# Kernel optimization log

Hardware: AMD Instinct MI355X
Metric: run time of the kernel (lower is better)

Reference implementation:

```python
import jax, jax.numpy as jnp
import numpy as np

N, C, H, E = 51200, 200, 128, 8
NE = N * 32
S_COEF, B_COEF = 0.01, 0.01
BN_EPS = 1e-5


def setup_inputs() -> dict:
    key = jax.random.key(0)
    ks = jax.random.split(key, 12)
    inp = {}
    inp["v"] = jax.random.normal(ks[0], (N, C), jnp.float32)
    inp["a_rows"] = jax.random.randint(ks[1], (NE,), 0, N, dtype=jnp.int32)
    inp["a_cols"] = jax.random.randint(ks[2], (NE,), 0, N, dtype=jnp.int32)
    inp["a_vals"] = jax.random.uniform(ks[3], (NE,), jnp.float32)
    inp["gate_W"] = jax.random.normal(ks[4], (C, E), jnp.float32) * 0.05
    inp["gate_b"] = jnp.zeros((E,), jnp.float32)
    inp["eps"] = jnp.zeros((E,), jnp.float32)  # GIN epsilon, init 0
    inp["W1"] = jax.random.normal(ks[5], (E, C, H), jnp.float32) / np.sqrt(C)
    inp["b1"] = jnp.zeros((E, H), jnp.float32)
    inp["g1"] = jnp.ones((E, H), jnp.float32)
    inp["beta1"] = jnp.zeros((E, H), jnp.float32)
    inp["W2"] = jax.random.normal(ks[6], (E, H, H), jnp.float32) / np.sqrt(H)
    inp["b2"] = jnp.zeros((E, H), jnp.float32)
    inp["g2"] = jnp.ones((E, H), jnp.float32)
    inp["beta2"] = jnp.zeros((E, H), jnp.float32)
    inp["b"] = 4
    inp["t"] = 64
    inp["n"] = 200
    return inp


def _bn_relu(h, g, beta):
    # h: [E, N, H]; batch-norm over node axis per expert (training-mode batch stats)
    mu = jnp.mean(h, axis=1, keepdims=True)
    var = jnp.var(h, axis=1, keepdims=True)
    hn = (h - mu) * jax.lax.rsqrt(var + BN_EPS)
    return jax.nn.relu(hn * g[:, None, :] + beta[:, None, :])


def reference(v, a_rows, a_cols, a_vals, gate_W, gate_b, eps,
              W1, b1, g1, beta1, W2, b2, g2, beta2, b, t, n):
    num_nodes, c = v.shape
    e = gate_W.shape[1]
    # ---- gating on x = rearrange(v, '(b t n) c -> b t n c') ----
    x = v.reshape(b, t, n, c)
    logits = jnp.einsum('btnc,ce->btne', x, gate_W) + gate_b
    probs = jax.nn.softmax(logits, axis=-1)                 # [b,t,n,E]
    top_val = jnp.max(probs, axis=-1, keepdims=True)
    top_idx = jnp.argmax(probs, axis=-1)
    gates = jax.nn.one_hot(top_idx, e, dtype=probs.dtype) * top_val  # top-1 sparse gates
    # ---- aux losses (switch-style balance; sparsity = mean top prob) ----
    probs_flat = probs.reshape(-1, e)
    gates_flat = gates.reshape(-1, e)
    importance = jnp.mean(probs_flat, axis=0)
    load = jnp.mean(jax.nn.one_hot(top_idx.reshape(-1), e, dtype=probs.dtype), axis=0)
    bal_loss = B_COEF * e * jnp.sum(importance * load)
    spa_loss = -S_COEF * jnp.mean(top_val)
    # ---- all-expert GIN compute (dense over experts, as in the torch loop) ----
    # shared sparse aggregation: agg[i] = sum_j a[i,j] * v[j]
    agg = jax.ops.segment_sum(a_vals[:, None] * v[a_cols], a_rows, num_segments=num_nodes)
    xin = agg[None] + (1.0 + eps)[:, None, None] * v[None]  # [E,N,C]
    h = jnp.einsum('enc,ech->enh', xin, W1) + b1[:, None, :]
    h = _bn_relu(h, g1, beta1)
    h = jnp.einsum('enk,ekh->enh', h, W2) + b2[:, None, :]
    h = _bn_relu(h, g2, beta2)                               # [E,N,H]
    # ---- gate-masked combine ----
    out = jnp.einsum('enh,ne->nh', h, gates_flat)            # [N,H]
    return out, (bal_loss, spa_loss)
```

## Files before the change

### kernel.cpp

```cpp
#include <hip/hip_runtime.h>


#define NNODES 51200
#define CDIM   200
#define CPAD   208
#define HDIM   128
#define NEXP   8
#define BNEPS  1e-5f
#define KC1    26
#define KS2    8
#define NB     400
#define CAP    6144
#define EPB    8192

typedef __attribute__((ext_vector_type(8)))  short short8;
typedef __attribute__((ext_vector_type(16))) float floatx16;
typedef unsigned short ushort_t;

__device__ __forceinline__ ushort_t f2bf(float x) {
  unsigned int u = __float_as_uint(x);
  u += 0x7fffu + ((u >> 16) & 1u);
  return (ushort_t)(u >> 16);
}
__device__ __forceinline__ float bf2f(ushort_t h) {
  return __uint_as_float(((unsigned int)h) << 16);
}

__global__ __launch_bounds__(256) void gating_kernel(
    const float* __restrict__ v, const float* __restrict__ gW,
    const float* __restrict__ gb, int* __restrict__ top_idx,
    float* __restrict__ top_val, ushort_t* __restrict__ v_bf,
    float* __restrict__ imp_acc, float* __restrict__ cnt_acc,
    float* __restrict__ tv_acc)
{
  __shared__ float s_imp[NEXP], s_cnt[NEXP], s_tv;
  const int tid = threadIdx.x, lane = tid & 63, wave = tid >> 6;
  if (tid < NEXP) { s_imp[tid] = 0.f; s_cnt[tid] = 0.f; }
  if (tid == 0) s_tv = 0.f;
  __syncthreads();
  const int c0 = lane * 4;
  const bool act = lane < 50;
  float gwr[4][NEXP];
#pragma unroll
  for (int r = 0; r < 4; ++r)
#pragma unroll
    for (int e = 0; e < NEXP; ++e)
      gwr[r][e] = act ? gW[(c0 + r) * NEXP + e] : 0.f;
  for (int i = 0; i < 16; ++i) {
    const int node = blockIdx.x * 64 + wave * 16 + i;
    float4 x = make_float4(0.f, 0.f, 0.f, 0.f);
    if (act) x = *(const float4*)(v + (size_t)node * CDIM + c0);
    float p[NEXP];
#pragma unroll
    for (int e = 0; e < NEXP; ++e)
      p[e] = fmaf(x.x, gwr[0][e],
             fmaf(x.y, gwr[1][e],
             fmaf(x.z, gwr[2][e], x.w * gwr[3][e])));
#pragma unroll
    for (int off = 32; off > 0; off >>= 1)
#pragma unroll
      for (int e = 0; e < NEXP; ++e) p[e] += __shfl_xor(p[e], off, 64);
#pragma unroll
    for (int e = 0; e < NEXP; ++e) p[e] += gb[e];
    if (lane < 52) {
      ushort4 o = {0, 0, 0, 0};
      if (act) { o.x = f2bf(x.x); o.y = f2bf(x.y); o.z = f2bf(x.z); o.w = f2bf(x.w); }
      *(ushort4*)(v_bf + (size_t)node * CPAD + c0) = o;
    }
    float mx = p[0]; int ai = 0;
#pragma unroll
    for (int e = 1; e < NEXP; ++e) if (p[e] > mx) { mx = p[e]; ai = e; }
    float se = 0.f, pe[NEXP];
#pragma unroll
    for (int e = 0; e < NEXP; ++e) { pe[e] = __expf(p[e] - mx); se += pe[e]; }
    const float inv = 1.f / se;
    if (lane == 0) {
      top_idx[node] = ai;
      top_val[node] = inv;
#pragma unroll
      for (int e = 0; e < NEXP; ++e) atomicAdd(&s_imp[e], pe[e] * inv);
      atomicAdd(&s_cnt[ai], 1.f);
      atomicAdd(&s_tv, inv);
    }
  }
  __syncthreads();
  if (tid < NEXP) { atomicAdd(&imp_acc[tid], s_imp[tid]); atomicAdd(&cnt_acc[tid], s_cnt[tid]); }
  if (tid == 0) atomicAdd(tv_acc, s_tv);
}

__global__ __launch_bounds__(256) void bucketA_kernel(
    const int* __restrict__ rows, const int* __restrict__ cols,
    const float* __restrict__ vals, int* __restrict__ bcnt,
    int2* __restrict__ tmp, int ne)
{
  __shared__ int cnt[NB];
  __shared__ int gbase[NB];
  const int tid = threadIdx.x;
  const int base = blockIdx.x * EPB;
  for (int b = tid; b < NB; b += 256) cnt[b] = 0;
  __syncthreads();
#pragma unroll 4
  for (int j = 0; j < EPB / 256; ++j) {
    const int i = base + j * 256 + tid;
    if (i < ne) atomicAdd(&cnt[rows[i] >> 7], 1);
  }
  __syncthreads();
  for (int b = tid; b < NB; b += 256) {
    const int c = cnt[b];
    gbase[b] = c ? (b * CAP + atomicAdd(&bcnt[b], c)) : 0;
    cnt[b] = 0;
  }
  __syncthreads();
#pragma unroll 4
  for (int j = 0; j < EPB / 256; ++j) {
    const int i = base + j * 256 + tid;
    if (i < ne) {
      const int r = rows[i];
      const int b = r >> 7;
      const int pos = gbase[b] + atomicAdd(&cnt[b], 1);
      tmp[pos] = make_int2((r << 16) | cols[i], __float_as_int(vals[i]));
    }
  }
}

__global__ __launch_bounds__(256) void bucketB_kernel(
    const int2* __restrict__ tmp, const int* __restrict__ bcnt,
    int2* __restrict__ cv, int* __restrict__ row_start, int* __restrict__ counts)
{
  __shared__ int lhist[128];
  __shared__ int lcur[128];
  const int tid = threadIdx.x;
  const int b = blockIdx.x;
  const int n = bcnt[b];
  const int base = b * CAP;
  int2 ed[CAP / 256];
#pragma unroll
  for (int j = 0; j < CAP / 256; ++j) {
    const int i = j * 256 + tid;
    if (i < n) ed[j] = tmp[base + i];
  }
  if (tid < 128) lhist[tid] = 0;
  __syncthreads();
#pragma unroll
  for (int j = 0; j < CAP / 256; ++j)
    if (j * 256 + tid < n)
      atomicAdd(&lhist[(((unsigned)ed[j].x) >> 16) & 127], 1);
  __syncthreads();
  if (tid == 0) {
    int acc = base;
    for (int r = 0; r < 128; ++r) { lcur[r] = acc; acc += lhist[r]; }
  }
  __syncthreads();
  if (tid < 128) {
    row_start[(b << 7) + tid] = lcur[tid];
    counts[(b << 7) + tid] = lhist[tid];
  }
  __syncthreads();
#pragma unroll
  for (int j = 0; j < CAP / 256; ++j)
    if (j * 256 + tid < n) {
      const int r = (((unsigned)ed[j].x) >> 16) & 127;
      const int pos = atomicAdd(&lcur[r], 1);
      cv[pos] = make_int2(ed[j].x & 0xffff, ed[j].y);
    }
}

__global__ __launch_bounds__(256) void aggregate_kernel(
    const ushort_t* __restrict__ v_bf, const int2* __restrict__ cv,
    const int* __restrict__ row_start, const int* __restrict__ counts,
    ushort_t* __restrict__ agg_bf)
{
  const int node = (blockIdx.x * 256 + threadIdx.x) >> 6;
  const int lane = threadIdx.x & 63;
  const int half = lane >> 5;
  const int l32  = lane & 31;
  const bool act = l32 < 26;
  const int start = row_start[node];
  const int cnt   = counts[node];

  float acc[8];
#pragma unroll
  for (int j = 0; j < 8; ++j) acc[j] = 0.f;

  int ecol = 0, eval = 0;
  if (lane < cnt) {
    const int2 e = cv[start + lane];
    ecol = e.x; eval = e.y;
  }
  const int n64 = cnt < 64 ? cnt : 64;
  int k = 0;

  for (; k + 16 <= n64; k += 16) {
    short8 xx[8];
#pragma unroll
    for (int u = 0; u < 8; ++u) {
      const int cc = __shfl(ecol, k + 2 * u + half, 64);
      short8 t = {0, 0, 0, 0, 0, 0, 0, 0};
      if (act) t = *(const short8*)(v_bf + (size_t)cc * CPAD + l32 * 8);
      xx[u] = t;
    }
#pragma unroll
    for (int u = 0; u < 8; ++u) {
      const float vv = __int_as_float(__shfl(eval, k + 2 * u + half, 64));
#pragma unroll
      for (int j = 0; j < 8; ++j)
        acc[j] = fmaf(vv, bf2f((ushort_t)xx[u][j]), acc[j]);
    }
  }
  for (; k + 4 <= n64; k += 4) {
    short8 xx[2];
#pragma unroll
    for (int u = 0; u < 2; ++u) {
      const int cc = __shfl(ecol, k + 2 * u + half, 64);
      short8 t = {0, 0, 0, 0, 0, 0, 0, 0};
      if (act) t = *(const short8*)(v_bf + (size_t)cc * CPAD + l32 * 8);
      xx[u] = t;
    }
#pragma unroll
    for (int u = 0; u < 2; ++u) {
      const float vv = __int_as_float(__shfl(eval, k + 2 * u + half, 64));
#pragma unroll
      for (int j = 0; j < 8; ++j)
        acc[j] = fmaf(vv, bf2f((ushort_t)xx[u][j]), acc[j]);
    }
  }
  for (; k < n64; k += 2) {
    const int idx = k + half;
    const int cc = __shfl(ecol, idx, 64);
    short8 t = {0, 0, 0, 0, 0, 0, 0, 0};
    if (act) t = *(const short8*)(v_bf + (size_t)cc * CPAD + l32 * 8);
    const float vv = __int_as_float(__shfl(eval, idx, 64));
#pragma unroll
    for (int j = 0; j < 8; ++j)
      acc[j] = fmaf(vv, bf2f((ushort_t)t[j]), acc[j]);
  }
  for (; k < cnt; ++k) {
    const int2 e0 = cv[start + k];
    short8 x0 = {0, 0, 0, 0, 0, 0, 0, 0};
    if (act && half == 0)
      x0 = *(const short8*)(v_bf + (size_t)e0.x * CPAD + l32 * 8);
    const float v0 = half ? 0.f : __int_as_float(e0.y);
#pragma unroll
    for (int j = 0; j < 8; ++j)
      acc[j] = fmaf(v0, bf2f((ushort_t)x0[j]), acc[j]);
  }

#pragma unroll
  for (int j = 0; j < 8; ++j) acc[j] += __shfl_xor(acc[j], 32, 64);

  if (act && half == 0) {
    short8 o;
#pragma unroll
    for (int j = 0; j < 8; ++j) o[j] = (short)f2bf(acc[j]);
    *(short8*)(agg_bf + (size_t)node * CPAD + l32 * 8) = o;
  }
}

__global__ __launch_bounds__(256) void btconv_all(
    const float* __restrict__ W1, const float* __restrict__ W2,
    const float* __restrict__ eps, ushort_t* __restrict__ Bt1,
    ushort_t* __restrict__ Bt2)
{
  const int e = blockIdx.y, j = blockIdx.x;
  __shared__ float tile[16][128];
  const int tid = threadIdx.x;
  const int kr = tid >> 5, n4 = (tid & 31) * 4;
  const float* W; int K, jj; float sc; ushort_t* dst;
  if (j < KC1) {
    sc = (j >= 13) ? (1.f + eps[e]) : 1.f;
    jj = (j >= 13) ? (j - 13) : j;
    W = W1; K = CDIM;
    dst = Bt1 + (((size_t)e * KC1 + j) * 256) * 8;
  } else {
    sc = 1.f; jj = j - KC1; W = W2; K = HDIM;
    dst = Bt2 + (((size_t)e * KS2 + jj) * 256) * 8;
  }
#pragma unroll
  for (int h = 0; h < 2; ++h) {
    const int k = jj * 16 + kr + h * 8;
    float4 val = make_float4(0.f, 0.f, 0.f, 0.f);
    if (k < K) val = *(const float4*)(W + ((size_t)e * K + k) * HDIM + n4);
    *(float4*)&tile[kr + h * 8][n4] = val;
  }
  __syncthreads();
  const int kh = tid >> 7, n = tid & 127;
  short8 pk;
#pragma unroll
  for (int q = 0; q < 8; ++q) pk[q] = (short)f2bf(sc * tile[kh * 8 + q][n]);
  *(short8*)(dst + (size_t)tid * 8) = pk;
}

__global__ __launch_bounds__(256, 2) void gemm1_mfma(
    const ushort_t* __restrict__ agg_bf, const ushort_t* __restrict__ v_bf,
    const ushort_t* __restrict__ Bt1x, ushort_t* __restrict__ h1,
    float* __restrict__ sum1, float* __restrict__ sq1)
{
  const int m0 = blockIdx.x * 64;
  __shared__ ushort_t sA[52 * 64 * 8];
  const int tid = threadIdx.x;
  const int lane = tid & 63, wid = tid >> 6;
  const int l31 = lane & 31, half = lane >> 5;

#pragma unroll
  for (int it = 0; it < 13; ++it) {
    const int l = it * 256 + tid;
    const int g = l >> 6, m = l & 63;
    const ushort_t* src = (g < 26)
        ? agg_bf + (size_t)(m0 + m) * CPAD + g * 8
        : v_bf  + (size_t)(m0 + m) * CPAD + (g - 26) * 8;
    *(short8*)(sA + (size_t)l * 8) = *(const short8*)src;
  }
  __syncthreads();

#pragma unroll
  for (int ei = 0; ei < 2; ++ei) {
    const int e = wid + ei * 4;
    floatx16 acc[2][4];
#pragma unroll
    for (int ms = 0; ms < 2; ++ms)
#pragma unroll
      for (int ns = 0; ns < 4; ++ns)
#pragma unroll
        for (int r = 0; r < 16; ++r) acc[ms][ns][r] = 0.f;

    const ushort_t* bte = Bt1x + ((size_t)e * KC1 * 256 + half * 128 + l31) * 8;
    short8 nb[4];
#pragma unroll
    for (int ns = 0; ns < 4; ++ns)
      nb[ns] = *(const short8*)(bte + (size_t)(ns * 32) * 8);
#pragma unroll
    for (int j = 0; j < KC1; ++j) {
      short8 b[4];
#pragma unroll
      for (int ns = 0; ns < 4; ++ns) b[ns] = nb[ns];
      if (j < KC1 - 1) {
#pragma unroll
        for (int ns = 0; ns < 4; ++ns)
          nb[ns] = *(const short8*)(bte + (size_t)((j + 1) * 256 + ns * 32) * 8);
      }
      short8 a[2];
#pragma unroll
      for (int ms = 0; ms < 2; ++ms)
        a[ms] = *(const short8*)(sA + (size_t)((2 * j + half) * 64 + ms * 32 + l31) * 8);
#pragma unroll
      for (int ms = 0; ms < 2; ++ms)
#pragma unroll
        for (int ns = 0; ns < 4; ++ns)
          acc[ms][ns] = __builtin_amdgcn_mfma_f32_32x32x16_bf16(
              a[ms], b[ns], acc[ms][ns], 0, 0, 0);
    }

    ushort_t* h1e = h1 + ((size_t)e * NNODES + m0) * HDIM;
#pragma unroll
    for (int ns = 0; ns < 4; ++ns) {
      const int col = ns * 32 + l31;
      float s = 0.f, q = 0.f;
#pragma unroll
      for (int ms = 0; ms < 2; ++ms) {
#pragma unroll
        for (int r = 0; r < 16; ++r) {
          const int row = ms * 32 + (r & 3) + 8 * (r >> 2) + 4 * half;
          const float x = acc[ms][ns][r];
          h1e[(size_t)row * HDIM + col] = f2bf(x);
          s += x; q = fmaf(x, x, q);
        }
      }
      s += __shfl_xor(s, 32, 64);
      q += __shfl_xor(q, 32, 64);
      if (half == 0) {
        atomicAdd(&sum1[e * HDIM + col], s);
        atomicAdd(&sq1[e * HDIM + col], q);
      }
    }
  }
}

__global__ __launch_bounds__(256, 4) void gemm2_mfma(
    const ushort_t* __restrict__ h1, const ushort_t* __restrict__ Bt2,
    const float* __restrict__ sum1, const float* __restrict__ sq1,
    const float* __restrict__ g1, const float* __restrict__ beta1,
    const int* __restrict__ top_idx, float* __restrict__ h2_sel,
    float* __restrict__ sum2, float* __restrict__ sq2)
{
  const int e = blockIdx.y;
  const int m0 = blockIdx.x * 128;
  __shared__ ushort_t sA[16 * 129 * 8];
  __shared__ float ssum[HDIM], ssq[HDIM];
  __shared__ float sSc[HDIM], sSh[HDIM];
  __shared__ int sTop[128];
  const int tid = threadIdx.x;
  const int lane = tid & 63, wid = tid >> 6;
  const int wm = wid >> 1, wn = wid & 1;
  const int l31 = lane & 31, half = lane >> 5;
  if (tid < HDIM) {
    ssum[tid] = 0.f; ssq[tid] = 0.f;
    sTop[tid] = top_idx[m0 + tid];
    const int i = e * HDIM + tid;
    const float invN = 1.f / (float)NNODES;
    const float mean = sum1[i] * invN;
    const float var  = sq1[i] * invN - mean * mean;
    const float sc = rsqrtf(var + BNEPS) * g1[i];
    sSc[tid] = sc;
    sSh[tid] = fmaf(-mean, sc, beta1[i]);
  }
  __syncthreads();
  {
    const int g = tid & 15, r0 = tid >> 4;
    const float4 sc0 = *(const float4*)&sSc[g * 8];
    const float4 sc1 = *(const float4*)&sSc[g * 8 + 4];
    const float4 sh0 = *(const float4*)&sSh[g * 8];
    const float4 sh1 = *(const float4*)&sSh[g * 8 + 4];
#pragma unroll
    for (int c = 0; c < 8; ++c) {
      const int m = c * 16 + r0;
      const short8 hq = *(const short8*)(
          h1 + ((size_t)e * NNODES + m0 + m) * HDIM + g * 8);
      short8 pk;
      pk[0] = (short)f2bf(fmaxf(0.f, fmaf(bf2f((ushort_t)hq[0]), sc0.x, sh0.x)));
      pk[1] = (short)f2bf(fmaxf(0.f, fmaf(bf2f((ushort_t)hq[1]), sc0.y, sh0.y)));
      pk[2] = (short)f2bf(fmaxf(0.f, fmaf(bf2f((ushort_t)hq[2]), sc0.z, sh0.z)));
      pk[3] = (short)f2bf(fmaxf(0.f, fmaf(bf2f((ushort_t)hq[3]), sc0.w, sh0.w)));
      pk[4] = (short)f2bf(fmaxf(0.f, fmaf(bf2f((ushort_t)hq[4]), sc1.x, sh1.x)));
      pk[5] = (short)f2bf(fmaxf(0.f, fmaf(bf2f((ushort_t)hq[5]), sc1.y, sh1.y)));
      pk[6] = (short)f2bf(fmaxf(0.f, fmaf(bf2f((ushort_t)hq[6]), sc1.z, sh1.z)));
      pk[7] = (short)f2bf(fmaxf(0.f, fmaf(bf2f((ushort_t)hq[7]), sc1.w, sh1.w)));
      *(short8*)(sA + (size_t)(g * 129 + m) * 8) = pk;
    }
  }
  __syncthreads();

  floatx16 acc[2][2];
#pragma unroll
  for (int i = 0; i < 2; ++i)
#pragma unroll
    for (int j = 0; j < 2; ++j)
#pragma unroll
      for (int r = 0; r < 16; ++r) acc[i][j][r] = 0.f;

  const ushort_t* bte = Bt2 + ((size_t)e * KS2 * 256 + half * 128 + wn * 64 + l31) * 8;
  short8 nb0 = *(const short8*)(bte);
  short8 nb1 = *(const short8*)(bte + 32 * 8);
#pragma unroll
  for (int ks = 0; ks < KS2; ++ks) {
    const short8 b0 = nb0, b1 = nb1;
    if (ks < KS2 - 1) {
      nb0 = *(const short8*)(bte + (size_t)((ks + 1) * 256) * 8);
      nb1 = *(const short8*)(bte + (size_t)((ks + 1) * 256 + 32) * 8);
    }
    const short8 a0 = *(const short8*)(sA + (size_t)((2 * ks + half) * 129 + wm * 64 + l31) * 8);
    const short8 a1 = *(const short8*)(sA + (size_t)((2 * ks + half) * 129 + wm * 64 + 32 + l31) * 8);
    acc[0][0] = __builtin_amdgcn_mfma_f32_32x32x16_bf16(a0, b0, acc[0][0], 0, 0, 0);
    acc[0][1] = __builtin_amdgcn_mfma_f32_32x32x16_bf16(a0, b1, acc[0][1], 0, 0, 0);
    acc[1][0] = __builtin_amdgcn_mfma_f32_32x32x16_bf16(a1, b0, acc[1][0], 0, 0, 0);
    acc[1][1] = __builtin_amdgcn_mfma_f32_32x32x16_bf16(a1, b1, acc[1][1], 0, 0, 0);
  }

#pragma unroll
  for (int ms = 0; ms < 2; ++ms)
#pragma unroll
    for (int ns = 0; ns < 2; ++ns) {
      const int col = wn * 64 + ns * 32 + l31;
      float s = 0.f, q = 0.f;
#pragma unroll
      for (int r = 0; r < 16; ++r) {
        const int row = wm * 64 + ms * 32 + (r & 3) + 8 * (r >> 2) + 4 * half;
        const float x = acc[ms][ns][r];
        if (sTop[row] == e) h2_sel[(size_t)(m0 + row) * HDIM + col] = x;
        s += x; q = fmaf(x, x, q);
      }
      atomicAdd(&ssum[col], s);
      atomicAdd(&ssq[col], q);
    }
  __syncthreads();
  if (tid < HDIM) atomicAdd(&sum2[e * HDIM + tid], ssum[tid]);
  else            atomicAdd(&sq2[e * HDIM + tid - HDIM], ssq[tid - HDIM]);
}

__global__ __launch_bounds__(256) void combine_kernel(
    const float* __restrict__ h2_sel, const int* __restrict__ top_idx,
    const float* __restrict__ top_val, const float* __restrict__ sum2,
    const float* __restrict__ sq2, const float* __restrict__ g2,
    const float* __restrict__ beta2, const float* __restrict__ imp,
    const float* __restrict__ cntv, const float* __restrict__ tv,
    float* __restrict__ out)
{
  __shared__ float s2[NEXP * HDIM], b2s[NEXP * HDIM];
  const int tid = threadIdx.x;
  const float invN = 1.f / (float)NNODES;
  for (int t = tid; t < NEXP * HDIM; t += 256) {
    const float mean = sum2[t] * invN;
    const float var  = sq2[t] * invN - mean * mean;
    const float sc = rsqrtf(var + BNEPS) * g2[t];
    s2[t] = sc;
    b2s[t] = fmaf(-mean, sc, beta2[t]);
  }
  __syncthreads();
  const int i4 = (blockIdx.x * 256 + tid) * 4;
  const int n = i4 >> 7, h = i4 & 127;
  const int e = top_idx[n];
  const float tvv = top_val[n];
  const float4 x = *(const float4*)(h2_sel + i4);
  const float* sc = s2 + e * HDIM + h;
  const float* sh = b2s + e * HDIM + h;
  float4 o;
  o.x = tvv * fmaxf(0.f, fmaf(x.x, sc[0], sh[0]));
  o.y = tvv * fmaxf(0.f, fmaf(x.y, sc[1], sh[1]));
  o.z = tvv * fmaxf(0.f, fmaf(x.z, sc[2], sh[2]));
  o.w = tvv * fmaxf(0.f, fmaf(x.w, sc[3], sh[3]));
  *(float4*)(out + i4) = o;
  if (blockIdx.x == 0 && tid == 0) {
    float bal = 0.f;
#pragma unroll
    for (int q = 0; q < NEXP; ++q) bal += (imp[q] * invN) * (cntv[q] * invN);
    out[(size_t)NNODES * HDIM]     = 0.01f * (float)NEXP * bal;
    out[(size_t)NNODES * HDIM + 1] = -0.01f * tv[0] * invN;
  }
}

struct WS {
  ushort_t *v_bf, *agg_bf, *h1, *Bt1x, *Bt2;
  float *h2_sel;
  int2 *cv, *tmp;
  int *row_start, *counts, *top_idx;
  float *top_val;
  char *zero_base; size_t zero_bytes;
  int *bcnt;
  float *sum1, *sq1, *sum2, *sq2, *imp, *cnt, *tv;
  size_t total;
};

static WS carve_ws(char* base)
{
  WS w; size_t off = 0;
  auto take = [&](size_t b) -> char* {
    char* r = base + off; off += (b + 255) & ~(size_t)255; return r;
  };
  w.v_bf   = (ushort_t*)take((size_t)NNODES * CPAD * 2);
  w.agg_bf = (ushort_t*)take((size_t)NNODES * CPAD * 2);
  w.h2_sel = (float*)w.v_bf;
  w.h1     = (ushort_t*)take((size_t)NEXP * NNODES * HDIM * 2);
  w.cv     = (int2*)take((size_t)NB * CAP * 8);
  w.tmp    = (int2*)take((size_t)NB * CAP * 8);
  w.Bt1x   = (ushort_t*)take((size_t)NEXP * KC1 * 2048 * 2);
  w.Bt2    = (ushort_t*)take((size_t)NEXP * KS2 * 2048 * 2);
  w.row_start = (int*)take(NNODES * 4);
  w.counts    = (int*)take(NNODES * 4);
  w.top_idx   = (int*)take(NNODES * 4);
  w.top_val   = (float*)take(NNODES * 4);
  w.zero_base = base + off;
  w.bcnt = (int*)take(NB * 4);
  w.sum1 = (float*)take(NEXP * HDIM * 4);
  w.sq1  = (float*)take(NEXP * HDIM * 4);
  w.sum2 = (float*)take(NEXP * HDIM * 4);
  w.sq2  = (float*)take(NEXP * HDIM * 4);
  w.imp  = (float*)take(NEXP * 4);
  w.cnt  = (float*)take(NEXP * 4);
  w.tv   = (float*)take(4);
  w.zero_bytes = (size_t)((base + off) - w.zero_base);
  w.total = off;
  return w;
}

extern "C" void kernel_launch(void* const* d_in, const int* in_sizes, int n_in,
                              void* d_out, int out_size, void* d_ws, size_t ws_size,
                              hipStream_t stream)
{
  const float* v      = (const float*)d_in[0];
  const int*   a_rows = (const int*)d_in[1];
  const int*   a_cols = (const int*)d_in[2];
  const float* a_vals = (const float*)d_in[3];
  const float* gate_W = (const float*)d_in[4];
  const float* gate_b = (const float*)d_in[5];
  const float* eps    = (const float*)d_in[6];
  const float* W1     = (const float*)d_in[7];
  const float* g1     = (const float*)d_in[9];
  const float* beta1  = (const float*)d_in[10];
  const float* W2     = (const float*)d_in[11];
  const float* g2     = (const float*)d_in[13];
  const float* beta2  = (const float*)d_in[14];
  const int NE = in_sizes[1];
  float* out = (float*)d_out;
  (void)n_in; (void)out_size; (void)ws_size;

  WS w = carve_ws((char*)d_ws);

  hipMemsetAsync(w.zero_base, 0, w.zero_bytes, stream);

  gating_kernel<<<NNODES / 64, 256, 0, stream>>>(
      v, gate_W, gate_b, w.top_idx, w.top_val, w.v_bf, w.imp, w.cnt, w.tv);
  btconv_all<<<dim3(KC1 + KS2, NEXP), 256, 0, stream>>>(
      W1, W2, eps, w.Bt1x, w.Bt2);
  bucketA_kernel<<<(NE + EPB - 1) / EPB, 256, 0, stream>>>(
      a_rows, a_cols, a_vals, w.bcnt, w.tmp, NE);
  bucketB_kernel<<<NB, 256, 0, stream>>>(
      w.tmp, w.bcnt, w.cv, w.row_start, w.counts);
  aggregate_kernel<<<NNODES / 4, 256, 0, stream>>>(
      w.v_bf, w.cv, w.row_start, w.counts, w.agg_bf);

  gemm1_mfma<<<NNODES / 64, 256, 0, stream>>>(
      w.agg_bf, w.v_bf, w.Bt1x, w.h1, w.sum1, w.sq1);
  gemm2_mfma<<<dim3(NNODES / 128, NEXP), 256, 0, stream>>>(
      w.h1, w.Bt2, w.sum1, w.sq1, g1, beta1, w.top_idx,
      w.h2_sel, w.sum2, w.sq2);
  combine_kernel<<<(NNODES * HDIM) / 1024, 256, 0, stream>>>(
      w.h2_sel, w.top_idx, w.top_val, w.sum2, w.sq2, g2, beta2,
      w.imp, w.cnt, w.tv, out);
}
```

Measured before the change: 517.7 us.

## Fuse sparse neighbor aggregation into gemm1 prologue, dropping agg buffer

The separate aggregate kernel is removed. gemm1 now gathers and sums neighbor rows of v_bf directly into its shared-memory A tile, each wave handling 16 nodes with the next node's edge list prefetched. This avoids writing and re-reading the bf16 agg array and one kernel launch. The cost is that the gather latency now sits inside the GEMM kernel, which runs at only 800 blocks with a 2-blocks-per-CU bound, so it has less parallelism to hide irregular memory accesses. The workspace for v_bf is also resized so it can still alias h2_sel.

```diff
diff --git a/kernel.cpp b/kernel.cpp
--- a/kernel.cpp
+++ b/kernel.cpp
@@ -163,97 +163,6 @@
       const int pos = atomicAdd(&lcur[r], 1);
       cv[pos] = make_int2(ed[j].x & 0xffff, ed[j].y);
     }
-}
-
-__global__ __launch_bounds__(256) void aggregate_kernel(
-    const ushort_t* __restrict__ v_bf, const int2* __restrict__ cv,
-    const int* __restrict__ row_start, const int* __restrict__ counts,
-    ushort_t* __restrict__ agg_bf)
-{
-  const int node = (blockIdx.x * 256 + threadIdx.x) >> 6;
-  const int lane = threadIdx.x & 63;
-  const int half = lane >> 5;
-  const int l32  = lane & 31;
-  const bool act = l32 < 26;
-  const int start = row_start[node];
-  const int cnt   = counts[node];
-
-  float acc[8];
-#pragma unroll
-  for (int j = 0; j < 8; ++j) acc[j] = 0.f;
-
-  int ecol = 0, eval = 0;
-  if (lane < cnt) {
-    const int2 e = cv[start + lane];
-    ecol = e.x; eval = e.y;
-  }
-  const int n64 = cnt < 64 ? cnt : 64;
-  int k = 0;
-
-  for (; k + 16 <= n64; k += 16) {
-    short8 xx[8];
-#pragma unroll
-    for (int u = 0; u < 8; ++u) {
-      const int cc = __shfl(ecol, k + 2 * u + half, 64);
-      short8 t = {0, 0, 0, 0, 0, 0, 0, 0};
-      if (act) t = *(const short8*)(v_bf + (size_t)cc * CPAD + l32 * 8);
-      xx[u] = t;
-    }
-#pragma unroll
-    for (int u = 0; u < 8; ++u) {
-      const float vv = __int_as_float(__shfl(eval, k + 2 * u + half, 64));
-#pragma unroll
-      for (int j = 0; j < 8; ++j)
-        acc[j] = fmaf(vv, bf2f((ushort_t)xx[u][j]), acc[j]);
-    }
-  }
-  for (; k + 4 <= n64; k += 4) {
-    short8 xx[2];
-#pragma unroll
-    for (int u = 0; u < 2; ++u) {
-      const int cc = __shfl(ecol, k + 2 * u + half, 64);
-      short8 t = {0, 0, 0, 0, 0, 0, 0, 0};
-      if (act) t = *(const short8*)(v_bf + (size_t)cc * CPAD + l32 * 8);
-      xx[u] = t;
-    }
-#pragma unroll
-    for (int u = 0; u < 2; ++u) {
-      const float vv = __int_as_float(__shfl(eval, k + 2 * u + half, 64));
-#pragma unroll
-      for (int j = 0; j < 8; ++j)
-        acc[j] = fmaf(vv, bf2f((ushort_t)xx[u][j]), acc[j]);
-    }
-  }
-  for (; k < n64; k += 2) {
-    const int idx = k + half;
-    const int cc = __shfl(ecol, idx, 64);
-    short8 t = {0, 0, 0, 0, 0, 0, 0, 0};
-    if (act) t = *(const short8*)(v_bf + (size_t)cc * CPAD + l32 * 8);
-    const float vv = __int_as_float(__shfl(eval, idx, 64));
-#pragma unroll
-    for (int j = 0; j < 8; ++j)
-      acc[j] = fmaf(vv, bf2f((ushort_t)t[j]), acc[j]);
-  }
-  for (; k < cnt; ++k) {
-    const int2 e0 = cv[start + k];
-    short8 x0 = {0, 0, 0, 0, 0, 0, 0, 0};
-    if (act && half == 0)
-      x0 = *(const short8*)(v_bf + (size_t)e0.x * CPAD + l32 * 8);
-    const float v0 = half ? 0.f : __int_as_float(e0.y);
-#pragma unroll
-    for (int j = 0; j < 8; ++j)
-      acc[j] = fmaf(v0, bf2f((ushort_t)x0[j]), acc[j]);
-  }
-
-#pragma unroll
-  for (int j = 0; j < 8; ++j) acc[j] += __shfl_xor(acc[j], 32, 64);
-
-  if (act && half == 0) {
-    short8 o;
-#pragma unroll
-    for (int j = 0; j < 8; ++j) o[j] = (short)f2bf(acc[j]);
-    *(short8*)(agg_bf + (size_t)node * CPAD + l32 * 8) = o;
-  }
 }
 
 __global__ __launch_bounds__(256) void btconv_all(
@@ -291,7 +200,8 @@
 }
 
 __global__ __launch_bounds__(256, 2) void gemm1_mfma(
-    const ushort_t* __restrict__ agg_bf, const ushort_t* __restrict__ v_bf,
+    const ushort_t* __restrict__ v_bf, const int2* __restrict__ cv,
+    const int* __restrict__ row_start, const int* __restrict__ counts,
     const ushort_t* __restrict__ Bt1x, ushort_t* __restrict__ h1,
     float* __restrict__ sum1, float* __restrict__ sq1)
 {
@@ -302,13 +212,109 @@
   const int l31 = lane & 31, half = lane >> 5;
 
 #pragma unroll
-  for (int it = 0; it < 13; ++it) {
+  for (int it = 0; it < 7; ++it) {
     const int l = it * 256 + tid;
-    const int g = l >> 6, m = l & 63;
-    const ushort_t* src = (g < 26)
-        ? agg_bf + (size_t)(m0 + m) * CPAD + g * 8
-        : v_bf  + (size_t)(m0 + m) * CPAD + (g - 26) * 8;
-    *(short8*)(sA + (size_t)l * 8) = *(const short8*)src;
+    if (l < 26 * 64) {
+      const int g = l >> 6, m = l & 63;
+      *(short8*)(sA + (size_t)((g + 26) * 64 + m) * 8) =
+          *(const short8*)(v_bf + (size_t)(m0 + m) * CPAD + g * 8);
+    }
+  }
+
+  {
+    const int l32 = lane & 31;
+    const int h2 = lane >> 5;
+    const bool gact = l32 < 26;
+    int rs16 = 0, ct16 = 0;
+    if (lane < 16) {
+      rs16 = row_start[m0 + wid * 16 + lane];
+      ct16 = counts[m0 + wid * 16 + lane];
+    }
+    int ecol = 0, eval = 0;
+    {
+      const int s0 = __shfl(rs16, 0, 64);
+      const int c0 = __shfl(ct16, 0, 64);
+      if (lane < c0) { const int2 e = cv[s0 + lane]; ecol = e.x; eval = e.y; }
+    }
+    for (int i = 0; i < 16; ++i) {
+      const int start = __shfl(rs16, i, 64);
+      const int cnt   = __shfl(ct16, i, 64);
+      int necol = 0, neval = 0;
+      if (i < 15) {
+        const int ns = __shfl(rs16, i + 1, 64);
+        const int nc = __shfl(ct16, i + 1, 64);
+        if (lane < nc) { const int2 e = cv[ns + lane]; necol = e.x; neval = e.y; }
+      }
+      float acc[8];
+#pragma unroll
+      for (int j = 0; j < 8; ++j) acc[j] = 0.f;
+      const int n64 = cnt < 64 ? cnt : 64;
+      int k = 0;
+      for (; k + 16 <= n64; k += 16) {
+        short8 xx[8];
+#pragma unroll
+        for (int u = 0; u < 8; ++u) {
+          const int cc = __shfl(ecol, k + 2 * u + h2, 64);
+          short8 t = {0, 0, 0, 0, 0, 0, 0, 0};
+          if (gact) t = *(const short8*)(v_bf + (size_t)cc * CPAD + l32 * 8);
+          xx[u] = t;
+        }
+#pragma unroll
+        for (int u = 0; u < 8; ++u) {
+          const float vv = __int_as_float(__shfl(eval, k + 2 * u + h2, 64));
+#pragma unroll
+          for (int j = 0; j < 8; ++j)
+            acc[j] = fmaf(vv, bf2f((ushort_t)xx[u][j]), acc[j]);
+        }
+      }
+      for (; k + 4 <= n64; k += 4) {
+        short8 xx[2];
+#pragma unroll
+        for (int u = 0; u < 2; ++u) {
+          const int cc = __shfl(ecol, k + 2 * u + h2, 64);
+          short8 t = {0, 0, 0, 0, 0, 0, 0, 0};
+          if (gact) t = *(const short8*)(v_bf + (size_t)cc * CPAD + l32 * 8);
+          xx[u] = t;
+        }
+#pragma unroll
+        for (int u = 0; u < 2; ++u) {
+          const float vv = __int_as_float(__shfl(eval, k + 2 * u + h2, 64));
+#pragma unroll
+          for (int j = 0; j < 8; ++j)
+            acc[j] = fmaf(vv, bf2f((ushort_t)xx[u][j]), acc[j]);
+        }
+      }
+      for (; k < n64; k += 2) {
+        const int idx = k + h2;
+        const int cc = __shfl(ecol, idx, 64);
+        short8 t = {0, 0, 0, 0, 0, 0, 0, 0};
+        if (gact) t = *(const short8*)(v_bf + (size_t)cc * CPAD + l32 * 8);
+        const float vv = __int_as_float(__shfl(eval, idx, 64));
+#pragma unroll
+        for (int j = 0; j < 8; ++j)
+          acc[j] = fmaf(vv, bf2f((ushort_t)t[j]), acc[j]);
+      }
+      for (; k < cnt; ++k) {
+        const int2 e0 = cv[start + k];
+        short8 x0 = {0, 0, 0, 0, 0, 0, 0, 0};
+        if (gact && h2 == 0)
+          x0 = *(const short8*)(v_bf + (size_t)e0.x * CPAD + l32 * 8);
+        const float v0 = h2 ? 0.f : __int_as_float(e0.y);
+#pragma unroll
+        for (int j = 0; j < 8; ++j)
+          acc[j] = fmaf(v0, bf2f((ushort_t)x0[j]), acc[j]);
+      }
+#pragma unroll
+      for (int j = 0; j < 8; ++j) acc[j] += __shfl_xor(acc[j], 32, 64);
+      if (gact && h2 == 0) {
+        short8 o;
+#pragma unroll
+        for (int j = 0; j < 8; ++j) o[j] = (short)f2bf(acc[j]);
+        const int m = wid * 16 + i;
+        *(short8*)(sA + (size_t)(l32 * 64 + m) * 8) = o;
+      }
+      ecol = necol; eval = neval;
+    }
   }
   __syncthreads();
 
@@ -518,7 +524,7 @@
 }
 
 struct WS {
-  ushort_t *v_bf, *agg_bf, *h1, *Bt1x, *Bt2;
+  ushort_t *v_bf, *h1, *Bt1x, *Bt2;
   float *h2_sel;
   int2 *cv, *tmp;
   int *row_start, *counts, *top_idx;
@@ -535,8 +541,7 @@
   auto take = [&](size_t b) -> char* {
     char* r = base + off; off += (b + 255) & ~(size_t)255; return r;
   };
-  w.v_bf   = (ushort_t*)take((size_t)NNODES * CPAD * 2);
-  w.agg_bf = (ushort_t*)take((size_t)NNODES * CPAD * 2);
+  w.v_bf   = (ushort_t*)take((size_t)NNODES * HDIM * 4);
   w.h2_sel = (float*)w.v_bf;
   w.h1     = (ushort_t*)take((size_t)NEXP * NNODES * HDIM * 2);
   w.cv     = (int2*)take((size_t)NB * CAP * 8);
@@ -594,11 +599,9 @@
       a_rows, a_cols, a_vals, w.bcnt, w.tmp, NE);
   bucketB_kernel<<<NB, 256, 0, stream>>>(
       w.tmp, w.bcnt, w.cv, w.row_start, w.counts);
-  aggregate_kernel<<<NNODES / 4, 256, 0, stream>>>(
-      w.v_bf, w.cv, w.row_start, w.counts, w.agg_bf);
 
   gemm1_mfma<<<NNODES / 64, 256, 0, stream>>>(
-      w.agg_bf, w.v_bf, w.Bt1x, w.h1, w.sum1, w.sq1);
+      w.v_bf, w.cv, w.row_start, w.counts, w.Bt1x, w.h1, w.sum1, w.sq1);
   gemm2_mfma<<<dim3(NNODES / 128, NEXP), 256, 0, stream>>>(
       w.h1, w.Bt2, w.sum1, w.sq1, g1, beta1, w.top_idx,
       w.h2_sel, w.sum2, w.sq2);
```

New measurement: 524.9 us. About the same (+1.4%).
